# Kernel tuning notes

Measured on AMD Instinct MI355X. Metric: run time of the kernel, lower is better.

Reference implementation:

```python
import jax, jax.numpy as jnp
import numpy as np

B, S, E, H = 2, 2048, 512, 8
HD = E // H  # head dim = 64


def setup_inputs() -> dict:
    key = jax.random.key(0)
    k1, k2, k3 = jax.random.split(key, 3)
    scale_qkv = (6.0 / (E + 3 * E)) ** 0.5  # xavier-uniform-like scale
    scale_o = (6.0 / (E + E)) ** 0.5
    return {
        "X": jax.random.normal(k1, (B, S, E), dtype=jnp.float32),
        "Wqkv": jax.random.uniform(k2, (E, 3 * E), jnp.float32, -scale_qkv, scale_qkv),
        "bqkv": jnp.zeros((3 * E,), jnp.float32),
        "Wo": jax.random.uniform(k3, (E, E), jnp.float32, -scale_o, scale_o),
        "bo": jnp.zeros((E,), jnp.float32),
    }


def reference(X, Wqkv, bqkv, Wo, bo):
    b, s, e = X.shape
    # qkv projection: [B,S,3E] -> [B,S,H,3*HD] -> [B,H,S,3*HD]
    qkv = X @ Wqkv + bqkv
    qkv = qkv.reshape(b, s, H, 3 * HD).transpose(0, 2, 1, 3)
    q, k, v = jnp.array_split(qkv, 3, axis=-1)  # each [B,H,S,HD]
    # naive scaled dot-product attention (full score matrix, per source)
    attn_logits = jnp.einsum("bhqd,bhkd->bhqk", q, k) / jnp.sqrt(jnp.float32(HD))
    attention = jax.nn.softmax(attn_logits, axis=-1)  # [B,H,S,S]
    values = jnp.einsum("bhqk,bhkd->bhqd", attention, v)
    values = values.transpose(0, 2, 1, 3).reshape(b, s, e)
    o = values @ Wo + bo
    return (o, attention)
```

## Files before the change

### kernel.cpp

```cpp
#include <hip/hip_runtime.h>

typedef unsigned short u16;
typedef u16 u16x2 __attribute__((ext_vector_type(2)));
typedef u16 u16x4 __attribute__((ext_vector_type(4)));
typedef u16 u16x8 __attribute__((ext_vector_type(8)));
typedef __bf16 bf16x8 __attribute__((ext_vector_type(8)));
typedef float f32x4 __attribute__((ext_vector_type(4)));
typedef float f32x2 __attribute__((ext_vector_type(2)));

#define MFMA16(A, B, C) __builtin_amdgcn_mfma_f32_16x16x32_bf16(A, B, C, 0, 0, 0)

#define SB 2
#define SS 2048
#define SE 512
#define SH 8
#define SHD 64

__device__ __forceinline__ u16 f2b(float f) {
  union { float f; unsigned u; } v;
  v.f = f;
  unsigned r = v.u + 0x7FFFu + ((v.u >> 16) & 1u);
  return (u16)(r >> 16);
}

__device__ __forceinline__ bf16x8 as_bf16x8(u16x8 v) {
  return __builtin_bit_cast(bf16x8, v);
}

__global__ __launch_bounds__(256, 4)
void qkv_kernel(const float* __restrict__ X, const float* __restrict__ W,
                const float* __restrict__ bias, u16* __restrict__ Q,
                u16* __restrict__ K, u16* __restrict__ Vt)
{
  __shared__ __align__(16) u16 As[64 * 32];
  __shared__ __align__(16) u16 Bs[64 * 40];
  const int tid  = threadIdx.x;
  const int lane = tid & 63, wave = tid >> 6, quad = lane >> 4, l16 = lane & 15;
  const int m0 = blockIdx.y * 64, n0 = blockIdx.x * 64;
  const int wr = (wave >> 1) * 32, wc = (wave & 1) * 32;
  const int arow = tid >> 2, acq = (tid & 3) * 4;
  const int bkr = tid >> 4, bnc = (tid & 15) * 4;

  const f32x4 z4 = {0.f, 0.f, 0.f, 0.f};
  f32x4 acc[2][2];
  acc[0][0] = z4; acc[0][1] = z4; acc[1][0] = z4; acc[1][1] = z4;

  for (int k0 = 0; k0 < 512; k0 += 32) {
    const float4 a0 = *(const float4*)&X[(m0 + arow) * 512 + k0 + acq];
    const float4 a1 = *(const float4*)&X[(m0 + arow) * 512 + k0 + 16 + acq];
    const float4 b0 = *(const float4*)&W[(k0 + bkr) * 1536 + n0 + bnc];
    const float4 b1 = *(const float4*)&W[(k0 + 16 + bkr) * 1536 + n0 + bnc];
    __syncthreads();
    u16x4 t0, t1;
    t0[0] = f2b(a0.x); t0[1] = f2b(a0.y); t0[2] = f2b(a0.z); t0[3] = f2b(a0.w);
    t1[0] = f2b(a1.x); t1[1] = f2b(a1.y); t1[2] = f2b(a1.z); t1[3] = f2b(a1.w);
    *(u16x4*)&As[arow * 32 + acq]      = t0;
    *(u16x4*)&As[arow * 32 + 16 + acq] = t1;
    Bs[(bnc + 0) * 40 + bkr]      = f2b(b0.x);
    Bs[(bnc + 1) * 40 + bkr]      = f2b(b0.y);
    Bs[(bnc + 2) * 40 + bkr]      = f2b(b0.z);
    Bs[(bnc + 3) * 40 + bkr]      = f2b(b0.w);
    Bs[(bnc + 0) * 40 + bkr + 16] = f2b(b1.x);
    Bs[(bnc + 1) * 40 + bkr + 16] = f2b(b1.y);
    Bs[(bnc + 2) * 40 + bkr + 16] = f2b(b1.z);
    Bs[(bnc + 3) * 40 + bkr + 16] = f2b(b1.w);
    __syncthreads();
    bf16x8 af0 = as_bf16x8(*(const u16x8*)&As[(wr + l16) * 32 + quad * 8]);
    bf16x8 af1 = as_bf16x8(*(const u16x8*)&As[(wr + 16 + l16) * 32 + quad * 8]);
    bf16x8 bf0 = as_bf16x8(*(const u16x8*)&Bs[(wc + l16) * 40 + quad * 8]);
    bf16x8 bf1 = as_bf16x8(*(const u16x8*)&Bs[(wc + 16 + l16) * 40 + quad * 8]);
    acc[0][0] = MFMA16(af0, bf0, acc[0][0]);
    acc[0][1] = MFMA16(af0, bf1, acc[0][1]);
    acc[1][0] = MFMA16(af1, bf0, acc[1][0]);
    acc[1][1] = MFMA16(af1, bf1, acc[1][1]);
  }

#pragma unroll
  for (int tm = 0; tm < 2; tm++) {
#pragma unroll
    for (int tn = 0; tn < 2; tn++) {
#pragma unroll
      for (int r = 0; r < 4; r++) {
        const int gm = m0 + wr + tm * 16 + quad * 4 + r;
        const int gn = n0 + wc + tn * 16 + l16;
        const float v = acc[tm][tn][r] + bias[gn];
        const int bb = gm >> 11, s = gm & 2047;
        const int hh = gn / 192, j = gn - hh * 192;
        const int bh = bb * SH + hh;
        if (j < 64)
          Q[(bh * SS + s) * SHD + j] = f2b(v * 0.125f);
        else if (j < 128)
          K[(bh * SS + s) * SHD + (j - 64)] = f2b(v);
        else
          Vt[(bh * SHD + (j - 128)) * SS + s] = f2b(v);
      }
    }
  }
}

__global__ __launch_bounds__(512, 2)
void attn_kernel(const u16* __restrict__ Q, const u16* __restrict__ K,
                 const u16* __restrict__ Vt, u16* __restrict__ values,
                 float* __restrict__ attn)
{
  __shared__ __align__(16) u16 p_lds[8 * 16 * 264];
  __shared__ float redmax[8][16];
  __shared__ float redsum[8][16];

  const int tid  = threadIdx.x;
  const int lane = tid & 63, wave = tid >> 6, quad = lane >> 4, l16 = lane & 15;
  const int q0 = blockIdx.x * 16;
  const int h = blockIdx.y, b = blockIdx.z, bh = b * SH + h;

  const u16* Qb = Q + bh * SS * SHD;
  const u16* Kb = K + bh * SS * SHD;
  const u16* Vb = Vt + bh * SHD * SS;

  const bf16x8 aq0 = as_bf16x8(*(const u16x8*)&Qb[(q0 + l16) * SHD + quad * 8]);
  const bf16x8 aq1 = as_bf16x8(*(const u16x8*)&Qb[(q0 + l16) * SHD + 32 + quad * 8]);

  f32x4 acc[16];
#pragma unroll
  for (int ct = 0; ct < 16; ct++) {
    const int kb = wave * 256 + ct * 16;
    bf16x8 bk0 = as_bf16x8(*(const u16x8*)&Kb[(kb + l16) * SHD + quad * 8]);
    bf16x8 bk1 = as_bf16x8(*(const u16x8*)&Kb[(kb + l16) * SHD + 32 + quad * 8]);
    f32x4 c = {0.f, 0.f, 0.f, 0.f};
    c = MFMA16(aq0, bk0, c);
    c = MFMA16(aq1, bk1, c);
    acc[ct] = c;
  }

  float mx[4];
#pragma unroll
  for (int r = 0; r < 4; r++) mx[r] = acc[0][r];
#pragma unroll
  for (int ct = 1; ct < 16; ct++)
#pragma unroll
    for (int r = 0; r < 4; r++) mx[r] = fmaxf(mx[r], acc[ct][r]);
#pragma unroll
  for (int off = 1; off < 16; off <<= 1)
#pragma unroll
    for (int r = 0; r < 4; r++) mx[r] = fmaxf(mx[r], __shfl_xor(mx[r], off));
  if (l16 == 0) {
#pragma unroll
    for (int r = 0; r < 4; r++) redmax[wave][quad * 4 + r] = mx[r];
  }
  __syncthreads();
  float gm[4];
#pragma unroll
  for (int r = 0; r < 4; r++) {
    float m = redmax[0][quad * 4 + r];
#pragma unroll
    for (int w = 1; w < 8; w++) m = fmaxf(m, redmax[w][quad * 4 + r]);
    gm[r] = m;
  }

  float ls[4] = {0.f, 0.f, 0.f, 0.f};
#pragma unroll
  for (int ct = 0; ct < 16; ct++)
#pragma unroll
    for (int r = 0; r < 4; r++) {
      const float p = __expf(acc[ct][r] - gm[r]);
      acc[ct][r] = p;
      ls[r] += p;
    }
#pragma unroll
  for (int off = 1; off < 16; off <<= 1)
#pragma unroll
    for (int r = 0; r < 4; r++) ls[r] += __shfl_xor(ls[r], off);
  if (l16 == 0) {
#pragma unroll
    for (int r = 0; r < 4; r++) redsum[wave][quad * 4 + r] = ls[r];
  }
  __syncthreads();
  float inv[4];
#pragma unroll
  for (int r = 0; r < 4; r++) {
    float s = redsum[0][quad * 4 + r];
#pragma unroll
    for (int w = 1; w < 8; w++) s += redsum[w][quad * 4 + r];
    inv[r] = 1.f / s;
  }

  float* attn_b = attn + (bh * SS + q0) * SS;
#pragma unroll
  for (int ct = 0; ct < 16; ct++) {
    const int col = wave * 256 + ct * 16 + l16;
#pragma unroll
    for (int r = 0; r < 4; r++) {
      const float p = acc[ct][r] * inv[r];
      attn_b[(quad * 4 + r) * SS + col] = p;
      p_lds[(wave * 16 + quad * 4 + r) * 264 + ct * 16 + l16] = f2b(p);
    }
  }

  f32x4 oacc[4];
#pragma unroll
  for (int nt = 0; nt < 4; nt++) oacc[nt] = (f32x4){0.f, 0.f, 0.f, 0.f};
#pragma unroll
  for (int kc = 0; kc < 8; kc++) {
    bf16x8 pa = as_bf16x8(*(const u16x8*)&p_lds[(wave * 16 + l16) * 264 + kc * 32 + quad * 8]);
    const int sb = wave * 256 + kc * 32 + quad * 8;
#pragma unroll
    for (int nt = 0; nt < 4; nt++) {
      bf16x8 vb = as_bf16x8(*(const u16x8*)&Vb[(nt * 16 + l16) * SS + sb]);
      oacc[nt] = MFMA16(pa, vb, oacc[nt]);
    }
  }

  __syncthreads();
  float* opart = (float*)p_lds;
#pragma unroll
  for (int nt = 0; nt < 4; nt++)
#pragma unroll
    for (int r = 0; r < 4; r++)
      opart[(wave * 16 + quad * 4 + r) * 64 + nt * 16 + l16] = oacc[nt][r];
  __syncthreads();

  const int q = tid >> 5, d0 = (tid & 31) * 2;
  f32x2 s2 = {0.f, 0.f};
#pragma unroll
  for (int w = 0; w < 8; w++) s2 += *(const f32x2*)&opart[(w * 16 + q) * 64 + d0];
  u16x2 o2;
  o2[0] = f2b(s2[0]);
  o2[1] = f2b(s2[1]);
  *(u16x2*)&values[((b * SS + q0 + q) * SH + h) * SHD + d0] = o2;
}

__global__ __launch_bounds__(256, 4)
void oproj_kernel(const u16* __restrict__ Vv, const float* __restrict__ W,
                  const float* __restrict__ bias, float* __restrict__ Out)
{
  __shared__ __align__(16) u16 As[64 * 32];
  __shared__ __align__(16) u16 Bs[64 * 40];
  const int tid  = threadIdx.x;
  const int lane = tid & 63, wave = tid >> 6, quad = lane >> 4, l16 = lane & 15;
  const int m0 = blockIdx.y * 64, n0 = blockIdx.x * 64;
  const int wr = (wave >> 1) * 32, wc = (wave & 1) * 32;
  const int arow = tid >> 2, acq = (tid & 3) * 8;
  const int bkr = tid >> 4, bnc = (tid & 15) * 4;

  const f32x4 z4 = {0.f, 0.f, 0.f, 0.f};
  f32x4 acc[2][2];
  acc[0][0] = z4; acc[0][1] = z4; acc[1][0] = z4; acc[1][1] = z4;

  for (int k0 = 0; k0 < 512; k0 += 32) {
    const u16x8 a = *(const u16x8*)&Vv[(m0 + arow) * 512 + k0 + acq];
    const float4 b0 = *(const float4*)&W[(k0 + bkr) * 512 + n0 + bnc];
    const float4 b1 = *(const float4*)&W[(k0 + 16 + bkr) * 512 + n0 + bnc];
    __syncthreads();
    *(u16x8*)&As[arow * 32 + acq] = a;
    Bs[(bnc + 0) * 40 + bkr]      = f2b(b0.x);
    Bs[(bnc + 1) * 40 + bkr]      = f2b(b0.y);
    Bs[(bnc + 2) * 40 + bkr]      = f2b(b0.z);
    Bs[(bnc + 3) * 40 + bkr]      = f2b(b0.w);
    Bs[(bnc + 0) * 40 + bkr + 16] = f2b(b1.x);
    Bs[(bnc + 1) * 40 + bkr + 16] = f2b(b1.y);
    Bs[(bnc + 2) * 40 + bkr + 16] = f2b(b1.z);
    Bs[(bnc + 3) * 40 + bkr + 16] = f2b(b1.w);
    __syncthreads();
    bf16x8 af0 = as_bf16x8(*(const u16x8*)&As[(wr + l16) * 32 + quad * 8]);
    bf16x8 af1 = as_bf16x8(*(const u16x8*)&As[(wr + 16 + l16) * 32 + quad * 8]);
    bf16x8 bf0 = as_bf16x8(*(const u16x8*)&Bs[(wc + l16) * 40 + quad * 8]);
    bf16x8 bf1 = as_bf16x8(*(const u16x8*)&Bs[(wc + 16 + l16) * 40 + quad * 8]);
    acc[0][0] = MFMA16(af0, bf0, acc[0][0]);
    acc[0][1] = MFMA16(af0, bf1, acc[0][1]);
    acc[1][0] = MFMA16(af1, bf0, acc[1][0]);
    acc[1][1] = MFMA16(af1, bf1, acc[1][1]);
  }

#pragma unroll
  for (int tm = 0; tm < 2; tm++)
#pragma unroll
    for (int tn = 0; tn < 2; tn++)
#pragma unroll
      for (int r = 0; r < 4; r++) {
        const int gm = m0 + wr + tm * 16 + quad * 4 + r;
        const int gn = n0 + wc + tn * 16 + l16;
        Out[gm * 512 + gn] = acc[tm][tn][r] + bias[gn];
      }
}

extern "C" void kernel_launch(void* const* d_in, const int* in_sizes, int n_in,
                              void* d_out, int out_size, void* d_ws, size_t ws_size,
                              hipStream_t stream) {
  const float* X    = (const float*)d_in[0];
  const float* Wqkv = (const float*)d_in[1];
  const float* bqkv = (const float*)d_in[2];
  const float* Wo   = (const float*)d_in[3];
  const float* bo   = (const float*)d_in[4];

  float* o_out    = (float*)d_out;
  float* attn_out = o_out + SB * SS * SE;

  const size_t QKV_ELEMS = (size_t)SB * SH * SS * SHD;
  u16* Q      = (u16*)d_ws;
  u16* K      = Q + QKV_ELEMS;
  u16* Vt     = K + QKV_ELEMS;
  u16* values = Vt + QKV_ELEMS;

  qkv_kernel<<<dim3(24, 64), 256, 0, stream>>>(X, Wqkv, bqkv, Q, K, Vt);
  attn_kernel<<<dim3(128, 8, 2), 512, 0, stream>>>(Q, K, Vt, values, attn_out);
  oproj_kernel<<<dim3(8, 64), 256, 0, stream>>>(values, Wo, bo, o_out);
}
```

Baseline: 455.8 us.

## Pre-convert X and weights to bf16, unify projections into 128x128-tile GEMM

Adds separate kernels that convert X to bf16 and transpose-convert the weight matrices to bf16 K-major layout, staged in scratch space (workspace and the attention output buffer). Both projections then use one templated GEMM with 128x128 tiles and a 4x4 MFMA grid per wave, in place of the old 64x64 tiles. The aim is to drop the per-tile fp32-to-bf16 conversion and the scattered transposed LDS stores, and to reuse each loaded tile across more MFMAs. In exchange it adds extra launches and memory passes, and with fewer blocks the smaller output projection may not fill the device.

```diff
diff --git a/kernel.cpp b/kernel.cpp
--- a/kernel.cpp
+++ b/kernel.cpp
@@ -27,72 +27,101 @@
   return __builtin_bit_cast(bf16x8, v);
 }
 
-__global__ __launch_bounds__(256, 4)
-void qkv_kernel(const float* __restrict__ X, const float* __restrict__ W,
-                const float* __restrict__ bias, u16* __restrict__ Q,
-                u16* __restrict__ K, u16* __restrict__ Vt)
-{
-  __shared__ __align__(16) u16 As[64 * 32];
-  __shared__ __align__(16) u16 Bs[64 * 40];
+__global__ __launch_bounds__(256)
+void convx_kernel(const float* __restrict__ X, u16* __restrict__ Xb)
+{
+  const int i = (blockIdx.x * 256 + threadIdx.x) * 4;
+  const float4 v = *(const float4*)&X[i];
+  u16x4 o;
+  o[0] = f2b(v.x); o[1] = f2b(v.y); o[2] = f2b(v.z); o[3] = f2b(v.w);
+  *(u16x4*)&Xb[i] = o;
+}
+
+__global__ __launch_bounds__(256)
+void wtrans_kernel(const float* __restrict__ in, u16* __restrict__ out, int N)
+{
+  __shared__ float t[32][33];
+  const int tid = threadIdx.x;
+  const int r = tid >> 3, c4 = (tid & 7) * 4;
+  const int k0 = blockIdx.y * 32, n0 = blockIdx.x * 32;
+  const float4 v = *(const float4*)&in[(size_t)(k0 + r) * N + n0 + c4];
+  t[r][c4 + 0] = v.x; t[r][c4 + 1] = v.y; t[r][c4 + 2] = v.z; t[r][c4 + 3] = v.w;
+  __syncthreads();
+  u16x4 o;
+  o[0] = f2b(t[c4 + 0][r]);
+  o[1] = f2b(t[c4 + 1][r]);
+  o[2] = f2b(t[c4 + 2][r]);
+  o[3] = f2b(t[c4 + 3][r]);
+  *(u16x4*)&out[(n0 + r) * 512 + k0 + c4] = o;
+}
+
+template <int MODE>
+__global__ __launch_bounds__(256, 2)
+void gemm_kernel(const u16* __restrict__ A, const u16* __restrict__ Bt,
+                 const float* __restrict__ bias,
+                 u16* __restrict__ Q, u16* __restrict__ K, u16* __restrict__ Vt,
+                 float* __restrict__ Out)
+{
+  __shared__ __align__(16) u16 As[128 * 40];
+  __shared__ __align__(16) u16 Bs[128 * 40];
   const int tid  = threadIdx.x;
   const int lane = tid & 63, wave = tid >> 6, quad = lane >> 4, l16 = lane & 15;
-  const int m0 = blockIdx.y * 64, n0 = blockIdx.x * 64;
-  const int wr = (wave >> 1) * 32, wc = (wave & 1) * 32;
-  const int arow = tid >> 2, acq = (tid & 3) * 4;
-  const int bkr = tid >> 4, bnc = (tid & 15) * 4;
+  const int m0 = blockIdx.y * 128, n0 = blockIdx.x * 128;
+  const int wr = (wave >> 1) * 64, wc = (wave & 1) * 64;
+  const int sr = tid >> 2, sc = (tid & 3) * 8;
 
   const f32x4 z4 = {0.f, 0.f, 0.f, 0.f};
-  f32x4 acc[2][2];
-  acc[0][0] = z4; acc[0][1] = z4; acc[1][0] = z4; acc[1][1] = z4;
+  f32x4 acc[4][4];
+#pragma unroll
+  for (int i = 0; i < 4; i++)
+#pragma unroll
+    for (int j = 0; j < 4; j++) acc[i][j] = z4;
 
   for (int k0 = 0; k0 < 512; k0 += 32) {
-    const float4 a0 = *(const float4*)&X[(m0 + arow) * 512 + k0 + acq];
-    const float4 a1 = *(const float4*)&X[(m0 + arow) * 512 + k0 + 16 + acq];
-    const float4 b0 = *(const float4*)&W[(k0 + bkr) * 1536 + n0 + bnc];
-    const float4 b1 = *(const float4*)&W[(k0 + 16 + bkr) * 1536 + n0 + bnc];
+    const u16x8 a0 = *(const u16x8*)&A[(m0 + sr) * 512 + k0 + sc];
+    const u16x8 a1 = *(const u16x8*)&A[(m0 + 64 + sr) * 512 + k0 + sc];
+    const u16x8 b0 = *(const u16x8*)&Bt[(n0 + sr) * 512 + k0 + sc];
+    const u16x8 b1 = *(const u16x8*)&Bt[(n0 + 64 + sr) * 512 + k0 + sc];
     __syncthreads();
-    u16x4 t0, t1;
-    t0[0] = f2b(a0.x); t0[1] = f2b(a0.y); t0[2] = f2b(a0.z); t0[3] = f2b(a0.w);
-    t1[0] = f2b(a1.x); t1[1] = f2b(a1.y); t1[2] = f2b(a1.z); t1[3] = f2b(a1.w);
-    *(u16x4*)&As[arow * 32 + acq]      = t0;
-    *(u16x4*)&As[arow * 32 + 16 + acq] = t1;
-    Bs[(bnc + 0) * 40 + bkr]      = f2b(b0.x);
-    Bs[(bnc + 1) * 40 + bkr]      = f2b(b0.y);
-    Bs[(bnc + 2) * 40 + bkr]      = f2b(b0.z);
-    Bs[(bnc + 3) * 40 + bkr]      = f2b(b0.w);
-    Bs[(bnc + 0) * 40 + bkr + 16] = f2b(b1.x);
-    Bs[(bnc + 1) * 40 + bkr + 16] = f2b(b1.y);
-    Bs[(bnc + 2) * 40 + bkr + 16] = f2b(b1.z);
-    Bs[(bnc + 3) * 40 + bkr + 16] = f2b(b1.w);
+    *(u16x8*)&As[sr * 40 + sc]        = a0;
+    *(u16x8*)&As[(64 + sr) * 40 + sc] = a1;
+    *(u16x8*)&Bs[sr * 40 + sc]        = b0;
+    *(u16x8*)&Bs[(64 + sr) * 40 + sc] = b1;
     __syncthreads();
-    bf16x8 af0 = as_bf16x8(*(const u16x8*)&As[(wr + l16) * 32 + quad * 8]);
-    bf16x8 af1 = as_bf16x8(*(const u16x8*)&As[(wr + 16 + l16) * 32 + quad * 8]);
-    bf16x8 bf0 = as_bf16x8(*(const u16x8*)&Bs[(wc + l16) * 40 + quad * 8]);
-    bf16x8 bf1 = as_bf16x8(*(const u16x8*)&Bs[(wc + 16 + l16) * 40 + quad * 8]);
-    acc[0][0] = MFMA16(af0, bf0, acc[0][0]);
-    acc[0][1] = MFMA16(af0, bf1, acc[0][1]);
-    acc[1][0] = MFMA16(af1, bf0, acc[1][0]);
-    acc[1][1] = MFMA16(af1, bf1, acc[1][1]);
-  }
-
-#pragma unroll
-  for (int tm = 0; tm < 2; tm++) {
-#pragma unroll
-    for (int tn = 0; tn < 2; tn++) {
+    bf16x8 af[4], bf[4];
+#pragma unroll
+    for (int i = 0; i < 4; i++) {
+      af[i] = as_bf16x8(*(const u16x8*)&As[(wr + i * 16 + l16) * 40 + quad * 8]);
+      bf[i] = as_bf16x8(*(const u16x8*)&Bs[(wc + i * 16 + l16) * 40 + quad * 8]);
+    }
+#pragma unroll
+    for (int i = 0; i < 4; i++)
+#pragma unroll
+      for (int j = 0; j < 4; j++) acc[i][j] = MFMA16(af[i], bf[j], acc[i][j]);
+  }
+
+#pragma unroll
+  for (int tm = 0; tm < 4; tm++) {
+#pragma unroll
+    for (int tn = 0; tn < 4; tn++) {
 #pragma unroll
       for (int r = 0; r < 4; r++) {
         const int gm = m0 + wr + tm * 16 + quad * 4 + r;
         const int gn = n0 + wc + tn * 16 + l16;
         const float v = acc[tm][tn][r] + bias[gn];
-        const int bb = gm >> 11, s = gm & 2047;
-        const int hh = gn / 192, j = gn - hh * 192;
-        const int bh = bb * SH + hh;
-        if (j < 64)
-          Q[(bh * SS + s) * SHD + j] = f2b(v * 0.125f);
-        else if (j < 128)
-          K[(bh * SS + s) * SHD + (j - 64)] = f2b(v);
-        else
-          Vt[(bh * SHD + (j - 128)) * SS + s] = f2b(v);
+        if (MODE == 0) {
+          const int bb = gm >> 11, s = gm & 2047;
+          const int hh = gn / 192, j = gn - hh * 192;
+          const int bh = bb * SH + hh;
+          if (j < 64)
+            Q[(bh * SS + s) * SHD + j] = f2b(v * 0.125f);
+          else if (j < 128)
+            K[(bh * SS + s) * SHD + (j - 64)] = f2b(v);
+          else
+            Vt[(bh * SHD + (j - 128)) * SS + s] = f2b(v);
+        } else {
+          Out[gm * 512 + gn] = v;
+        }
       }
     }
   }
@@ -228,60 +257,6 @@
   *(u16x2*)&values[((b * SS + q0 + q) * SH + h) * SHD + d0] = o2;
 }
 
-__global__ __launch_bounds__(256, 4)
-void oproj_kernel(const u16* __restrict__ Vv, const float* __restrict__ W,
-                  const float* __restrict__ bias, float* __restrict__ Out)
-{
-  __shared__ __align__(16) u16 As[64 * 32];
-  __shared__ __align__(16) u16 Bs[64 * 40];
-  const int tid  = threadIdx.x;
-  const int lane = tid & 63, wave = tid >> 6, quad = lane >> 4, l16 = lane & 15;
-  const int m0 = blockIdx.y * 64, n0 = blockIdx.x * 64;
-  const int wr = (wave >> 1) * 32, wc = (wave & 1) * 32;
-  const int arow = tid >> 2, acq = (tid & 3) * 8;
-  const int bkr = tid >> 4, bnc = (tid & 15) * 4;
-
-  const f32x4 z4 = {0.f, 0.f, 0.f, 0.f};
-  f32x4 acc[2][2];
-  acc[0][0] = z4; acc[0][1] = z4; acc[1][0] = z4; acc[1][1] = z4;
-
-  for (int k0 = 0; k0 < 512; k0 += 32) {
-    const u16x8 a = *(const u16x8*)&Vv[(m0 + arow) * 512 + k0 + acq];
-    const float4 b0 = *(const float4*)&W[(k0 + bkr) * 512 + n0 + bnc];
-    const float4 b1 = *(const float4*)&W[(k0 + 16 + bkr) * 512 + n0 + bnc];
-    __syncthreads();
-    *(u16x8*)&As[arow * 32 + acq] = a;
-    Bs[(bnc + 0) * 40 + bkr]      = f2b(b0.x);
-    Bs[(bnc + 1) * 40 + bkr]      = f2b(b0.y);
-    Bs[(bnc + 2) * 40 + bkr]      = f2b(b0.z);
-    Bs[(bnc + 3) * 40 + bkr]      = f2b(b0.w);
-    Bs[(bnc + 0) * 40 + bkr + 16] = f2b(b1.x);
-    Bs[(bnc + 1) * 40 + bkr + 16] = f2b(b1.y);
-    Bs[(bnc + 2) * 40 + bkr + 16] = f2b(b1.z);
-    Bs[(bnc + 3) * 40 + bkr + 16] = f2b(b1.w);
-    __syncthreads();
-    bf16x8 af0 = as_bf16x8(*(const u16x8*)&As[(wr + l16) * 32 + quad * 8]);
-    bf16x8 af1 = as_bf16x8(*(const u16x8*)&As[(wr + 16 + l16) * 32 + quad * 8]);
-    bf16x8 bf0 = as_bf16x8(*(const u16x8*)&Bs[(wc + l16) * 40 + quad * 8]);
-    bf16x8 bf1 = as_bf16x8(*(const u16x8*)&Bs[(wc + 16 + l16) * 40 + quad * 8]);
-    acc[0][0] = MFMA16(af0, bf0, acc[0][0]);
-    acc[0][1] = MFMA16(af0, bf1, acc[0][1]);
-    acc[1][0] = MFMA16(af1, bf0, acc[1][0]);
-    acc[1][1] = MFMA16(af1, bf1, acc[1][1]);
-  }
-
-#pragma unroll
-  for (int tm = 0; tm < 2; tm++)
-#pragma unroll
-    for (int tn = 0; tn < 2; tn++)
-#pragma unroll
-      for (int r = 0; r < 4; r++) {
-        const int gm = m0 + wr + tm * 16 + quad * 4 + r;
-        const int gn = n0 + wc + tn * 16 + l16;
-        Out[gm * 512 + gn] = acc[tm][tn][r] + bias[gn];
-      }
-}
-
 extern "C" void kernel_launch(void* const* d_in, const int* in_sizes, int n_in,
                               void* d_out, int out_size, void* d_ws, size_t ws_size,
                               hipStream_t stream) {
@@ -299,8 +274,16 @@
   u16* K      = Q + QKV_ELEMS;
   u16* Vt     = K + QKV_ELEMS;
   u16* values = Vt + QKV_ELEMS;
-
-  qkv_kernel<<<dim3(24, 64), 256, 0, stream>>>(X, Wqkv, bqkv, Q, K, Vt);
+  u16* Xb     = values;
+  u16* WqkvT  = (u16*)attn_out;
+  u16* WoT    = Q;
+
+  convx_kernel<<<dim3(2048), 256, 0, stream>>>(X, Xb);
+  wtrans_kernel<<<dim3(48, 16), 256, 0, stream>>>(Wqkv, WqkvT, 1536);
+
+  gemm_kernel<0><<<dim3(12, 32), 256, 0, stream>>>(Xb, WqkvT, bqkv, Q, K, Vt, nullptr);
   attn_kernel<<<dim3(128, 8, 2), 512, 0, stream>>>(Q, K, Vt, values, attn_out);
-  oproj_kernel<<<dim3(8, 64), 256, 0, stream>>>(values, Wo, bo, o_out);
-}
+  wtrans_kernel<<<dim3(16, 16), 256, 0, stream>>>(Wo, WoT, 512);
+  gemm_kernel<1><<<dim3(4, 32), 256, 0, stream>>>(values, WoT, bo,
+                                                  nullptr, nullptr, nullptr, o_out);
+}
```

New measurement: 441.2 us. -3.2%, faster.
